# Kernel tuning notes

Hardware: AMD Instinct MI355X
Metric: run time of the kernel (lower is better)

Reference implementation:

```python
import jax, jax.numpy as jnp
import numpy as np

B, N, IN_DIM = 256, 300, 1280
DIM, DEPTH, HEADS = 256, 2, 4
DIM_HEAD = DIM // HEADS            # 64
NB_FEAT = int(DIM_HEAD * np.log(DIM_HEAD))  # 266, lucidrains default
FF_HIDDEN = 4 * DIM
LN_EPS = 1e-5
KERNEL_EPS = 1e-4


def _orthogonal_random_matrix(nb_rows, nb_cols, rng):
    # gaussian orthogonal random matrix, scaling=0 (chi-norm multipliers)
    blocks = []
    full = nb_rows // nb_cols
    for _ in range(full):
        q, _ = np.linalg.qr(rng.standard_normal((nb_cols, nb_cols)))
        blocks.append(q.T)
    rem = nb_rows - full * nb_cols
    if rem:
        q, _ = np.linalg.qr(rng.standard_normal((nb_cols, nb_cols)))
        blocks.append(q.T[:rem])
    mat = np.concatenate(blocks, 0)
    mult = np.linalg.norm(rng.standard_normal((nb_rows, nb_cols)), axis=1)
    return (mult[:, None] * mat).astype(np.float32)


def setup_inputs() -> dict:
    key = jax.random.key(0)
    ks = jax.random.split(key, 24)
    s = 0.02
    rng = np.random.default_rng(0)
    proj = jnp.asarray(np.stack([_orthogonal_random_matrix(NB_FEAT, DIM_HEAD, rng)
                                 for _ in range(DEPTH)]))  # [L, M, dh]
    return {
        "x": jax.random.normal(ks[0], (B, N, IN_DIM), jnp.float32),
        "w_in": jax.random.normal(ks[1], (IN_DIM, DIM), jnp.float32) * s,
        "b_in": jnp.zeros((DIM,), jnp.float32),
        "proj": proj,
        "ln1_g": jnp.ones((DEPTH, DIM), jnp.float32),
        "ln1_b": jnp.zeros((DEPTH, DIM), jnp.float32),
        "wq": jax.random.normal(ks[2], (DEPTH, DIM, DIM), jnp.float32) * s,
        "wk": jax.random.normal(ks[3], (DEPTH, DIM, DIM), jnp.float32) * s,
        "wv": jax.random.normal(ks[4], (DEPTH, DIM, DIM), jnp.float32) * s,
        "wo": jax.random.normal(ks[5], (DEPTH, DIM, DIM), jnp.float32) * s,
        "bo": jnp.zeros((DEPTH, DIM), jnp.float32),
        "ln2_g": jnp.ones((DEPTH, DIM), jnp.float32),
        "ln2_b": jnp.zeros((DEPTH, DIM), jnp.float32),
        "w1": jax.random.normal(ks[6], (DEPTH, DIM, FF_HIDDEN), jnp.float32) * s,
        "b1": jnp.zeros((DEPTH, FF_HIDDEN), jnp.float32),
        "w2": jax.random.normal(ks[7], (DEPTH, FF_HIDDEN, DIM), jnp.float32) * s,
        "b2": jnp.zeros((DEPTH, DIM), jnp.float32),
        "hln_g": jnp.ones((DIM,), jnp.float32),
        "hln_b": jnp.zeros((DIM,), jnp.float32),
        "wh1": jax.random.normal(ks[8], (DIM, 128), jnp.float32) * s,
        "bh1": jnp.zeros((128,), jnp.float32),
        "wh2": jax.random.normal(ks[9], (128, 1), jnp.float32) * s,
        "bh2": jnp.zeros((1,), jnp.float32),
    }


def _layernorm(x, g, b):
    mu = jnp.mean(x, -1, keepdims=True)
    var = jnp.mean(jnp.square(x - mu), -1, keepdims=True)
    return (x - mu) * jax.lax.rsqrt(var + LN_EPS) * g + b


def _softmax_kernel(data, proj, is_query):
    # data: [b,h,n,dh], proj: [m,dh] -> features [b,h,n,m] (FAVOR+ positive softmax kernel)
    norm = DIM_HEAD ** -0.25
    ratio = proj.shape[0] ** -0.5
    dd = jnp.einsum('bhnd,md->bhnm', data * norm, proj)
    diag = 0.5 * jnp.sum(jnp.square(data), -1) * (norm ** 2)  # [b,h,n]
    if is_query:
        stab = jnp.max(dd, axis=-1, keepdims=True)
    else:
        stab = jnp.max(dd, axis=(-2, -1), keepdims=True)
    return ratio * (jnp.exp(dd - diag[..., None] - stab) + KERNEL_EPS)


def _linear_attention(q, k, v, proj):
    # non-causal FAVOR+: O(n*m*d) instead of O(n^2*d)
    qp = _softmax_kernel(q, proj, True)    # [b,h,n,m]
    kp = _softmax_kernel(k, proj, False)   # [b,h,n,m]
    d_inv = 1.0 / jnp.einsum('bhnm,bhm->bhn', qp, jnp.sum(kp, axis=-2))
    context = jnp.einsum('bhnm,bhnd->bhmd', kp, v)
    return jnp.einsum('bhnm,bhmd->bhnd', qp, context) * d_inv[..., None]


def reference(x, w_in, b_in, proj, ln1_g, ln1_b, wq, wk, wv, wo, bo,
              ln2_g, ln2_b, w1, b1, w2, b2, hln_g, hln_b, wh1, bh1, wh2, bh2):
    h = x @ w_in + b_in                                   # [B,N,DIM]
    for l in range(DEPTH):
        # --- pre-norm FAVOR+ self-attention ---
        y = _layernorm(h, ln1_g[l], ln1_b[l])
        q = (y @ wq[l]).reshape(B, N, HEADS, DIM_HEAD).transpose(0, 2, 1, 3)
        k = (y @ wk[l]).reshape(B, N, HEADS, DIM_HEAD).transpose(0, 2, 1, 3)
        v = (y @ wv[l]).reshape(B, N, HEADS, DIM_HEAD).transpose(0, 2, 1, 3)
        o = _linear_attention(q, k, v, proj[l])
        o = o.transpose(0, 2, 1, 3).reshape(B, N, DIM)
        h = h + (o @ wo[l] + bo[l])
        # --- pre-norm FFN (GELU, mult=4) ---
        y = _layernorm(h, ln2_g[l], ln2_b[l])
        h = h + (jax.nn.gelu(y @ w1[l] + b1[l]) @ w2[l] + b2[l])
    pooled = jnp.mean(h, axis=1)                          # [B,DIM]
    z = _layernorm(pooled, hln_g, hln_b)
    z = jax.nn.relu(z @ wh1 + bh1)
    return jax.nn.sigmoid(z @ wh2 + bh2)                  # [B,1]
```

## Files before the change

kernel.cpp:

```cpp
#include <hip/hip_runtime.h>
#include <hip/hip_bf16.h>


#define MF 266
#define NSEQ 300
#define DIMC 256
#define NORM_QK 0.3535533905932738f
#define KEPS 1e-4f

typedef __attribute__((ext_vector_type(8))) short bf16x8;
typedef __attribute__((ext_vector_type(4))) float f32x4;

#define MFMA16(a, b, c) __builtin_amdgcn_mfma_f32_16x16x32_bf16((a), (b), (c), 0, 0, 0)

__device__ __forceinline__ float bfbits2f(ushort u) {
  return __uint_as_float(((unsigned int)u) << 16);
}
__device__ __forceinline__ ushort f2us(float f) {
  __hip_bfloat16 b = __float2bfloat16(f);
  return *(ushort*)&b;
}
__device__ __forceinline__ float sq8(uint4 u) {
  float s = 0.f;
  const unsigned int uu[4] = {u.x, u.y, u.z, u.w};
#pragma unroll
  for (int i = 0; i < 4; i++) {
    const float a = bfbits2f((ushort)(uu[i] & 0xffff));
    const float b = bfbits2f((ushort)(uu[i] >> 16));
    s += a * a + b * b;
  }
  return s;
}
__device__ __forceinline__ void gld16(const void* g, void* l) {
  __builtin_amdgcn_global_load_lds(
      (const __attribute__((address_space(1))) unsigned int*)g,
      (__attribute__((address_space(3))) unsigned int*)l, 16, 0, 0);
}
__device__ __forceinline__ float fast_gelu(float x) {
  const float t = 0.7978845608028654f * (x + 0.044715f * x * x * x);
  const float e = __expf(2.0f * fabsf(t));
  float th = 1.0f - 2.0f / (e + 1.0f);
  th = (t < 0.0f) ? -th : th;
  return 0.5f * x * (1.0f + th);
}

template<int EPI, int OUTBF, int AF32>
__global__ __launch_bounds__(256) void gemm_mfma(
    const ushort* __restrict__ A, const float* __restrict__ Af,
    const ushort* __restrict__ BT,
    const float* __restrict__ bias, const float* __restrict__ R,
    float* __restrict__ Cf, __hip_bfloat16* __restrict__ Cb,
    ushort* __restrict__ Cq, int M, int N, int K)
{
  __shared__ ushort As[128][32];
  __shared__ ushort Bs[128][32];
  const int tid = threadIdx.x;
  const int row0 = blockIdx.x << 7, col0 = blockIdx.y << 7;
  const int w = tid >> 6, lane = tid & 63;
  const int wm = (w >> 1) << 6, wn = (w & 1) << 6;
  const int r = lane & 15, quad = lane >> 4;
  const int sr = tid >> 2, sc = (tid & 3) << 3;
  f32x4 acc[4][4];
#pragma unroll
  for (int i = 0; i < 4; i++)
#pragma unroll
    for (int j = 0; j < 4; j++) acc[i][j] = (f32x4){0.f, 0.f, 0.f, 0.f};
  const ushort* ap0 = A + (size_t)(row0 + sr) * K + sc;
  const ushort* ap1 = A + (size_t)(row0 + sr + 64) * K + sc;
  const float*  af0 = Af + (size_t)(row0 + sr) * K + sc;
  const float*  af1 = Af + (size_t)(row0 + sr + 64) * K + sc;
  const ushort* bp0 = BT + (size_t)(col0 + sr) * K + sc;
  const ushort* bp1 = BT + (size_t)(col0 + sr + 64) * K + sc;
  for (int k0 = 0; k0 < K; k0 += 32) {
    if (AF32) {
      const float4 u0 = *(const float4*)(af0 + k0);
      const float4 u1 = *(const float4*)(af0 + k0 + 4);
      const float4 u2 = *(const float4*)(af1 + k0);
      const float4 u3 = *(const float4*)(af1 + k0 + 4);
      ushort4 p0, p1, p2, p3;
      p0.x=f2us(u0.x); p0.y=f2us(u0.y); p0.z=f2us(u0.z); p0.w=f2us(u0.w);
      p1.x=f2us(u1.x); p1.y=f2us(u1.y); p1.z=f2us(u1.z); p1.w=f2us(u1.w);
      p2.x=f2us(u2.x); p2.y=f2us(u2.y); p2.z=f2us(u2.z); p2.w=f2us(u2.w);
      p3.x=f2us(u3.x); p3.y=f2us(u3.y); p3.z=f2us(u3.z); p3.w=f2us(u3.w);
      *(ushort4*)&As[sr][sc]      = p0;
      *(ushort4*)&As[sr][sc+4]    = p1;
      *(ushort4*)&As[sr+64][sc]   = p2;
      *(ushort4*)&As[sr+64][sc+4] = p3;
    } else {
      gld16(ap0 + k0, &As[sr][sc]);
      gld16(ap1 + k0, &As[sr + 64][sc]);
    }
    gld16(bp0 + k0, &Bs[sr][sc]);
    gld16(bp1 + k0, &Bs[sr + 64][sc]);
    __syncthreads();
    bf16x8 af[4], bfv[4];
#pragma unroll
    for (int i = 0; i < 4; i++) af[i]  = *(const bf16x8*)&As[wm + i*16 + r][quad << 3];
#pragma unroll
    for (int i = 0; i < 4; i++) bfv[i] = *(const bf16x8*)&Bs[wn + i*16 + r][quad << 3];
#pragma unroll
    for (int mi = 0; mi < 4; mi++)
#pragma unroll
      for (int ni = 0; ni < 4; ni++)
        acc[mi][ni] = MFMA16(af[mi], bfv[ni], acc[mi][ni]);
    __syncthreads();
  }
#pragma unroll
  for (int mi = 0; mi < 4; mi++) {
    const int rowb = row0 + wm + mi*16 + (quad << 2);
#pragma unroll
    for (int ni = 0; ni < 4; ni++) {
      const int col = col0 + wn + ni*16 + r;
      if (EPI == 4) {
        const int tsel = col >> 8, hd = col & 255, hh = hd >> 6, d = hd & 63;
        const float sc_ = (tsel == 2) ? 1.f : NORM_QK;
#pragma unroll
        for (int j = 0; j < 4; j++) {
          const int rowj = rowb + j;
          const int bq = rowj / 300, nq = rowj - bq * 300;
          Cq[(((size_t)tsel * 1024 + (bq << 2) + hh) * 300 + nq) * 64 + d] =
              f2us(acc[mi][ni][j] * sc_);
        }
      } else {
        const float bv = bias[col];
#pragma unroll
        for (int j = 0; j < 4; j++) {
          const size_t off = (size_t)(rowb + j) * N + col;
          float vv = acc[mi][ni][j] + bv;
          if (EPI == 1) vv += R[off];
          if (EPI == 2) vv = fast_gelu(vv);
          if (OUTBF) Cb[off] = __float2bfloat16(vv);
          else       Cf[off] = vv;
        }
      }
    }
  }
}

__global__ __launch_bounds__(256) void cast_bf16_kernel(
    const float* __restrict__ in, ushort* __restrict__ out, int n4)
{
  const int i = blockIdx.x * 256 + threadIdx.x;
  if (i >= n4) return;
  const float4 v = ((const float4*)in)[i];
  ushort4 rr;
  rr.x = f2us(v.x); rr.y = f2us(v.y); rr.z = f2us(v.z); rr.w = f2us(v.w);
  ((ushort4*)out)[i] = rr;
}

struct TSeg { const float* src; ushort* dst; int R; int C; int base; };
struct TTab { TSeg s[13]; };
__global__ __launch_bounds__(256) void tcast_all(TTab tab) {
  __shared__ float t[32][33];
  const int bid = blockIdx.x;
  int si = 0;
#pragma unroll
  for (int i = 1; i < 13; i++) if (bid >= tab.s[i].base) si = i;
  const float* src = tab.s[si].src;
  ushort* dst = tab.s[si].dst;
  const int R = tab.s[si].R, C = tab.s[si].C;
  const int local = bid - tab.s[si].base;
  const int cw = C >> 5;
  const int c0 = (local % cw) << 5, r0 = (local / cw) << 5;
  const int tx = threadIdx.x & 31, ty = threadIdx.x >> 5;
#pragma unroll
  for (int i = 0; i < 32; i += 8)
    t[ty + i][tx] = src[(size_t)(r0 + ty + i) * C + c0 + tx];
  __syncthreads();
#pragma unroll
  for (int i = 0; i < 32; i += 8)
    dst[(size_t)(c0 + ty + i) * R + r0 + tx] = f2us(t[tx][ty + i]);
}

__global__ __launch_bounds__(256) void ln_kernel(
    const float* __restrict__ x, const float* __restrict__ g,
    const float* __restrict__ b, __hip_bfloat16* __restrict__ y)
{
  const int wid = threadIdx.x >> 6, lane = threadIdx.x & 63;
  const int row = blockIdx.x * 4 + wid;
  const float* xr = x + (size_t)row * DIMC;
  float v[4];
  float s = 0.f;
#pragma unroll
  for (int i = 0; i < 4; i++) { v[i] = xr[lane + 64*i]; s += v[i]; }
#pragma unroll
  for (int off = 32; off; off >>= 1) s += __shfl_xor(s, off);
  const float mu = s * (1.0f/256.0f);
  float var = 0.f;
#pragma unroll
  for (int i = 0; i < 4; i++) { const float d = v[i] - mu; var += d*d; }
#pragma unroll
  for (int off = 32; off; off >>= 1) var += __shfl_xor(var, off);
  const float rstd = rsqrtf(var * (1.0f/256.0f) + 1e-5f);
  __hip_bfloat16* yr = y + (size_t)row * DIMC;
#pragma unroll
  for (int i = 0; i < 4; i++) {
    const int c = lane + 64*i;
    yr[c] = __float2bfloat16((v[i] - mu) * rstd * g[c] + b[c]);
  }
}

__global__ __launch_bounds__(512) void favor_fused_kernel(
    const ushort* __restrict__ qn_all, const ushort* __restrict__ kn_all,
    const ushort* __restrict__ v_all, const ushort* __restrict__ projb,
    ushort* __restrict__ Ob)
{
  __shared__ __align__(16) uint8_t smem[151424];
  ushort (*kn_s)[72]      = (ushort(*)[72])(smem);
  ushort (*vT_s)[328]     = (ushort(*)[328])(smem + 46080);
  ushort (*proj_s)[72]    = (ushort(*)[72])(smem + 88064);
  ushort (*kpT_s)[40]     = (ushort(*)[40])(smem + 127232);
  ushort (*qp_s)[16][72]  = (ushort(*)[16][72])(smem + 127232);
  float* diag_s = (float*)(smem + 148992);
  float* ksum_s = (float*)(smem + 150272);
  float* red_s  = (float*)(smem + 151360);

  const int tid = threadIdx.x, w = tid >> 6, lane = tid & 63;
  const int bh = blockIdx.x;
  const int b = bh >> 2, h = bh & 3;
  const int r = lane & 15, quad = lane >> 4;
  const int rl = lane >> 3, c8 = lane & 7;

  {
    const ushort* knb = kn_all + (size_t)bh * 19200;
    for (int row = w*8 + rl; row < 320; row += 64) {
      uint4 u = {0u,0u,0u,0u};
      if (row < 300) u = *(const uint4*)(knb + row*64 + c8*8);
      *(uint4*)&kn_s[row][c8*8] = u;
      float s = sq8(u);
      s += __shfl_xor(s, 1); s += __shfl_xor(s, 2); s += __shfl_xor(s, 4);
      if (c8 == 0) diag_s[row] = 0.5f * s;
    }
    const ushort* vb = v_all + (size_t)bh * 19200;
    for (int row = w*8 + rl; row < 328; row += 64) {
      uint4 u = {0u,0u,0u,0u};
      if (row < 300) u = *(const uint4*)(vb + row*64 + c8*8);
      const unsigned int uu[4] = {u.x, u.y, u.z, u.w};
#pragma unroll
      for (int p = 0; p < 4; p++) {
        vT_s[c8*8 + 2*p    ][row] = (ushort)(uu[p] & 0xffff);
        vT_s[c8*8 + 2*p + 1][row] = (ushort)(uu[p] >> 16);
      }
    }
    for (int row = w*8 + rl; row < 272; row += 64) {
      uint4 u = {0u,0u,0u,0u};
      if (row < 266) u = *(const uint4*)(projb + row*64 + c8*8);
      *(uint4*)&proj_s[row][c8*8] = u;
    }
  }
  __syncthreads();

  f32x4 cacc[9];
#pragma unroll
  for (int i = 0; i < 9; i++) cacc[i] = (f32x4){0.f,0.f,0.f,0.f};
  float ksum_acc = 0.f;
  float stab = -3.0e38f;

  for (int c = 0; c < 10; c++) {
    f32x4 ddreg[5];
    float cmax = -3.0e38f;
#pragma unroll
    for (int ii = 0; ii < 5; ii++) {
      const int t = w + ii*8;
      if (t < 34) {
        const int tm = t >> 1, tn = c*2 + (t & 1);
        const bf16x8 a0 = *(const bf16x8*)&proj_s[tm*16 + r][quad*8];
        const bf16x8 a1 = *(const bf16x8*)&proj_s[tm*16 + r][32 + quad*8];
        const bf16x8 b0 = *(const bf16x8*)&kn_s[tn*16 + r][quad*8];
        const bf16x8 b1 = *(const bf16x8*)&kn_s[tn*16 + r][32 + quad*8];
        f32x4 acc = (f32x4){0.f,0.f,0.f,0.f};
        acc = MFMA16(a0, b0, acc);
        acc = MFMA16(a1, b1, acc);
        ddreg[ii] = acc;
        const int n = tn*16 + r;
        if (n < 300) {
#pragma unroll
          for (int j = 0; j < 4; j++) {
            const int m = tm*16 + quad*4 + j;
            if (m < 266) cmax = fmaxf(cmax, acc[j]);
          }
        }
      }
    }
#pragma unroll
    for (int off = 32; off; off >>= 1) cmax = fmaxf(cmax, __shfl_xor(cmax, off));
    if (lane == 0) red_s[w] = cmax;
    __syncthreads();
    float bmax = red_s[0];
#pragma unroll
    for (int i = 1; i < 8; i++) bmax = fmaxf(bmax, red_s[i]);
    const float stab_new = fmaxf(stab, bmax);
    const float alpha = __expf(stab - stab_new);
    stab = stab_new;
    ksum_acc *= alpha;
#pragma unroll
    for (int i = 0; i < 9; i++)
#pragma unroll
      for (int j = 0; j < 4; j++) cacc[i][j] *= alpha;
#pragma unroll
    for (int ii = 0; ii < 5; ii++) {
      const int t = w + ii*8;
      if (t < 34) {
        const int tm = t >> 1, tnl = t & 1, tn = c*2 + tnl;
        const int n = tn*16 + r;
        const float dgn = diag_s[n];
#pragma unroll
        for (int j = 0; j < 4; j++) {
          const int m = tm*16 + quad*4 + j;
          float kp = 0.f;
          if (n < 300 && m < 266) kp = __expf(ddreg[ii][j] - dgn - stab) + KEPS;
          kpT_s[m][tnl*16 + r] = f2us(kp);
        }
      }
    }
    __syncthreads();
    if (tid < 272) {
      float rs = 0.f;
#pragma unroll
      for (int kk = 0; kk < 4; kk++) {
        const uint4 u = *(const uint4*)&kpT_s[tid][kk*8];
        const unsigned int uu[4] = {u.x, u.y, u.z, u.w};
#pragma unroll
        for (int p = 0; p < 4; p++)
          rs += bfbits2f((ushort)(uu[p] & 0xffff)) + bfbits2f((ushort)(uu[p] >> 16));
      }
      ksum_acc += rs;
    }
#pragma unroll
    for (int ii = 0; ii < 9; ii++) {
      const int t2 = w + ii*8;
      if (t2 < 68) {
        const int tm = t2 >> 2, td = t2 & 3;
        const bf16x8 aa = *(const bf16x8*)&kpT_s[tm*16 + r][quad*8];
        const bf16x8 bb = *(const bf16x8*)&vT_s[td*16 + r][c*32 + quad*8];
        cacc[ii] = MFMA16(aa, bb, cacc[ii]);
      }
    }
    __syncthreads();
  }

  if (tid < 272) ksum_s[tid] = ksum_acc;
#pragma unroll
  for (int ii = 0; ii < 9; ii++) {
    const int t2 = w + ii*8;
    if (t2 < 68) {
      const int tm = t2 >> 2, td = t2 & 3;
#pragma unroll
      for (int j = 0; j < 4; j++) {
        const int m = tm*16 + quad*4 + j;
        vT_s[td*16 + r][m] = f2us(cacc[ii][j]);
      }
    }
  }
  {
    const ushort* qb = qn_all + (size_t)bh * 19200;
    for (int row = w*8 + rl; row < 320; row += 64) {
      uint4 u = {0u,0u,0u,0u};
      if (row < 300) u = *(const uint4*)(qb + row*64 + c8*8);
      *(uint4*)&kn_s[row][c8*8] = u;
      float s = sq8(u);
      s += __shfl_xor(s, 1); s += __shfl_xor(s, 2); s += __shfl_xor(s, 4);
      if (c8 == 0) diag_s[row] = 0.5f * s;
    }
  }
  __syncthreads();

  for (int t = w; t < 19; t += 8) {
    const bf16x8 a0 = *(const bf16x8*)&kn_s[t*16 + r][quad*8];
    const bf16x8 a1 = *(const bf16x8*)&kn_s[t*16 + r][32 + quad*8];
    f32x4 dd[17];
#pragma unroll
    for (int tm = 0; tm < 17; tm++) {
      const bf16x8 b0 = *(const bf16x8*)&proj_s[tm*16 + r][quad*8];
      const bf16x8 b1 = *(const bf16x8*)&proj_s[tm*16 + r][32 + quad*8];
      f32x4 acc = (f32x4){0.f,0.f,0.f,0.f};
      acc = MFMA16(a0, b0, acc);
      acc = MFMA16(a1, b1, acc);
      dd[tm] = acc;
    }
    float mxj[4] = {-3.0e38f, -3.0e38f, -3.0e38f, -3.0e38f};
#pragma unroll
    for (int tm = 0; tm < 17; tm++) {
      if (tm*16 + r < 266) {
#pragma unroll
        for (int j = 0; j < 4; j++) mxj[j] = fmaxf(mxj[j], dd[tm][j]);
      }
    }
#pragma unroll
    for (int off = 1; off < 16; off <<= 1)
#pragma unroll
      for (int j = 0; j < 4; j++) mxj[j] = fmaxf(mxj[j], __shfl_xor(mxj[j], off));
    float dg[4];
#pragma unroll
    for (int j = 0; j < 4; j++) dg[j] = diag_s[t*16 + quad*4 + j];
    float den[4] = {0.f, 0.f, 0.f, 0.f};
#pragma unroll
    for (int tm = 0; tm < 17; tm++) {
      const float ks = ksum_s[tm*16 + r];
      const bool mval = (tm*16 + r < 266);
#pragma unroll
      for (int j = 0; j < 4; j++) {
        const int n = t*16 + quad*4 + j;
        float qp = 0.f;
        if (mval && n < 300) qp = __expf(dd[tm][j] - dg[j] - mxj[j]) + KEPS;
        dd[tm][j] = qp;
        den[j] += qp * ks;
      }
    }
#pragma unroll
    for (int off = 1; off < 16; off <<= 1)
#pragma unroll
      for (int j = 0; j < 4; j++) den[j] += __shfl_xor(den[j], off);
    float dinv[4];
#pragma unroll
    for (int j = 0; j < 4; j++) dinv[j] = 1.0f / den[j];

    f32x4 oacc[4];
#pragma unroll
    for (int td = 0; td < 4; td++) oacc[td] = (f32x4){0.f,0.f,0.f,0.f};
#pragma unroll
    for (int g = 0; g < 5; g++) {
#pragma unroll
      for (int tt = 0; tt < 4; tt++) {
        const int tm = g*4 + tt;
#pragma unroll
        for (int j = 0; j < 4; j++) {
          const ushort us = (tm <= 16) ? f2us(dd[tm][j]) : (ushort)0;
          qp_s[w][quad*4 + j][tt*16 + r] = us;
        }
      }
#pragma unroll
      for (int s = 0; s < 2; s++) {
        const bf16x8 aa = *(const bf16x8*)&qp_s[w][r][s*32 + quad*8];
#pragma unroll
        for (int td = 0; td < 4; td++) {
          const bf16x8 bb = *(const bf16x8*)&vT_s[td*16 + r][g*64 + s*32 + quad*8];
          oacc[td] = MFMA16(aa, bb, oacc[td]);
        }
      }
    }
#pragma unroll
    for (int td = 0; td < 4; td++) {
#pragma unroll
      for (int j = 0; j < 4; j++) {
        const int n = t*16 + quad*4 + j;
        if (n < 300)
          Ob[((size_t)b*300 + n)*256 + h*64 + td*16 + r] = f2us(oacc[td][j] * dinv[j]);
      }
    }
  }
}

__global__ __launch_bounds__(256) void head_kernel(
    const float* __restrict__ h, const float* __restrict__ hg,
    const float* __restrict__ hb, const float* __restrict__ wh1,
    const float* __restrict__ bh1, const float* __restrict__ wh2,
    const float* __restrict__ bh2, float* __restrict__ out)
{
  __shared__ float z_s[256];
  __shared__ float hid_s[128];
  __shared__ float red_s[4];
  const int b = blockIdx.x, tid = threadIdx.x;
  const float* hb_ = h + (size_t)b * NSEQ * DIMC;
  float s = 0.f;
  for (int n = 0; n < NSEQ; n++) s += hb_[(size_t)n * DIMC + tid];
  s *= (1.0f / 300.0f);
  float t1 = s;
#pragma unroll
  for (int off = 32; off; off >>= 1) t1 += __shfl_xor(t1, off);
  if ((tid & 63) == 0) red_s[tid >> 6] = t1;
  __syncthreads();
  const float mu = (red_s[0] + red_s[1] + red_s[2] + red_s[3]) * (1.0f/256.0f);
  __syncthreads();
  const float d = s - mu;
  float vv = d * d;
#pragma unroll
  for (int off = 32; off; off >>= 1) vv += __shfl_xor(vv, off);
  if ((tid & 63) == 0) red_s[tid >> 6] = vv;
  __syncthreads();
  const float var = (red_s[0] + red_s[1] + red_s[2] + red_s[3]) * (1.0f/256.0f);
  z_s[tid] = d * rsqrtf(var + 1e-5f) * hg[tid] + hb[tid];
  __syncthreads();
  if (tid < 128) {
    float acc = bh1[tid];
    for (int dd = 0; dd < 256; dd++) acc += z_s[dd] * wh1[dd * 128 + tid];
    hid_s[tid] = fmaxf(acc, 0.f);
  }
  __syncthreads();
  if (tid < 64) {
    float acc = hid_s[tid] * wh2[tid] + hid_s[tid + 64] * wh2[tid + 64];
#pragma unroll
    for (int off = 32; off; off >>= 1) acc += __shfl_xor(acc, off);
    if (tid == 0) {
      const float val = acc + bh2[0];
      out[b] = 1.0f / (1.0f + __expf(-val));
    }
  }
}

extern "C" void kernel_launch(void* const* d_in, const int* in_sizes, int n_in,
                              void* d_out, int out_size, void* d_ws, size_t ws_size,
                              hipStream_t stream) {
  const float* x    = (const float*)d_in[0];
  const float* w_in = (const float*)d_in[1];
  const float* b_in = (const float*)d_in[2];
  const float* proj = (const float*)d_in[3];
  const float* ln1g = (const float*)d_in[4];
  const float* ln1b = (const float*)d_in[5];
  const float* wq   = (const float*)d_in[6];
  const float* wk   = (const float*)d_in[7];
  const float* wv   = (const float*)d_in[8];
  const float* wo   = (const float*)d_in[9];
  const float* bo   = (const float*)d_in[10];
  const float* ln2g = (const float*)d_in[11];
  const float* ln2b = (const float*)d_in[12];
  const float* w1   = (const float*)d_in[13];
  const float* b1   = (const float*)d_in[14];
  const float* w2   = (const float*)d_in[15];
  const float* b2   = (const float*)d_in[16];
  const float* hg   = (const float*)d_in[17];
  const float* hbp  = (const float*)d_in[18];
  const float* wh1  = (const float*)d_in[19];
  const float* bh1  = (const float*)d_in[20];
  const float* wh2  = (const float*)d_in[21];
  const float* bh2  = (const float*)d_in[22];

  uint8_t* base = (uint8_t*)d_ws;
  float*  h     = (float*)(base);
  ushort* yb    = (ushort*)(base + 78643200);
  ushort* qkv   = (ushort*)(base + 117964800);
  ushort* ob    = (ushort*)(base + 235929600);
  ushort* wbuf  = (ushort*)(base + 275251200);
  ushort* projb = (ushort*)(base + 279052288);
  ushort* tb = qkv;
  ushort* qb = qkv;
  ushort* kb = qkv + 19660800;
  ushort* vb = qkv + 39321600;

  ushort* w_inT = wbuf;
  ushort* wT0   = wbuf + 327680;

  cast_bf16_kernel<<<34, 256, 0, stream>>>(proj, projb, 8512);
  TTab tab;
  int nb = 0;
  auto add = [&](const float* s, ushort* d, int R, int C) {
    tab.s[nb % 13] = TSeg{s, d, R, C, 0};
  };
  {
    int idx = 0, basem = 0;
    auto seg = [&](const float* s, ushort* d, int R, int C) {
      tab.s[idx] = TSeg{s, d, R, C, basem};
      basem += (R >> 5) * (C >> 5);
      idx++;
    };
    seg(w_in, w_inT, 1280, 256);
    for (int l = 0; l < 2; l++) {
      ushort* wl = wT0 + (size_t)l * 786432;
      seg(wq + (size_t)l*65536,  wl,          256, 256);
      seg(wk + (size_t)l*65536,  wl + 65536,  256, 256);
      seg(wv + (size_t)l*65536,  wl + 131072, 256, 256);
      seg(wo + (size_t)l*65536,  wl + 196608, 256, 256);
      seg(w1 + (size_t)l*262144, wl + 262144, 256, 1024);
      seg(w2 + (size_t)l*262144, wl + 524288, 1024, 256);
    }
    nb = basem;
  }
  tcast_all<<<nb, 256, 0, stream>>>(tab);

  gemm_mfma<0,0,1><<<dim3(600, 2), 256, 0, stream>>>(
      nullptr, x, w_inT, b_in, nullptr, h, nullptr, nullptr, 76800, 256, 1280);

  for (int l = 0; l < 2; l++) {
    ushort* wl = wT0 + (size_t)l * 786432;
    ushort* projL = projb + (size_t)l * 17024;
    ln_kernel<<<19200, 256, 0, stream>>>(h, ln1g + l*256, ln1b + l*256, (__hip_bfloat16*)yb);
    gemm_mfma<4,0,0><<<dim3(600, 6), 256, 0, stream>>>(
        yb, nullptr, wl, nullptr, nullptr, nullptr, nullptr, qkv, 76800, 768, 256);
    favor_fused_kernel<<<1024, 512, 0, stream>>>(qb, kb, vb, projL, ob);
    gemm_mfma<1,0,0><<<dim3(600, 2), 256, 0, stream>>>(
        ob, nullptr, wl + 196608, bo + l*256, h, h, nullptr, nullptr, 76800, 256, 256);
    ln_kernel<<<19200, 256, 0, stream>>>(h, ln2g + l*256, ln2b + l*256, (__hip_bfloat16*)yb);
    gemm_mfma<2,1,0><<<dim3(600, 8), 256, 0, stream>>>(
        yb, nullptr, wl + 262144, b1 + l*1024, nullptr, nullptr, (__hip_bfloat16*)tb, nullptr, 76800, 1024, 256);
    gemm_mfma<1,0,0><<<dim3(600, 2), 256, 0, stream>>>(
        tb, nullptr, wl + 524288, b2 + l*256, h, h, nullptr, nullptr, 76800, 256, 1024);
  }
  head_kernel<<<256, 256, 0, stream>>>(h, hg, hbp, wh1, bh1, wh2, bh2, (float*)d_out);
}
```

Measured before the change: 1.790 ms.

## Fuse LN2, FFN up-projection with GELU, and down-projection into one kernel

```diff
diff --git a/kernel.cpp b/kernel.cpp
--- a/kernel.cpp
+++ b/kernel.cpp
@@ -55,7 +55,7 @@
   __shared__ ushort As[128][32];
   __shared__ ushort Bs[128][32];
   const int tid = threadIdx.x;
-  const int row0 = blockIdx.x << 7, col0 = blockIdx.y << 7;
+  const int row0 = blockIdx.y << 7, col0 = blockIdx.x << 7;
   const int w = tid >> 6, lane = tid & 63;
   const int wm = (w >> 1) << 6, wn = (w & 1) << 6;
   const int r = lane & 15, quad = lane >> 4;
@@ -128,10 +128,131 @@
           const size_t off = (size_t)(rowb + j) * N + col;
           float vv = acc[mi][ni][j] + bv;
           if (EPI == 1) vv += R[off];
-          if (EPI == 2) vv = fast_gelu(vv);
           if (OUTBF) Cb[off] = __float2bfloat16(vv);
           else       Cf[off] = vv;
         }
+      }
+    }
+  }
+}
+
+__global__ __launch_bounds__(512, 4) void ffn_fused_kernel(
+    float* __restrict__ h, const ushort* __restrict__ w1T,
+    const float* __restrict__ b1, const ushort* __restrict__ w2T,
+    const float* __restrict__ b2, const float* __restrict__ lng,
+    const float* __restrict__ lnb)
+{
+  __shared__ ushort Ys[64][264];
+  __shared__ ushort Hs[64][136];
+  const int tid = threadIdx.x, w = tid >> 6, lane = tid & 63;
+  const int r = lane & 15, quad = lane >> 4;
+  const int row0 = blockIdx.x << 6;
+
+  {
+    const int rl = lane >> 3, c8 = lane & 7;
+    const int row = (w << 3) + rl;
+    const float4* h4 = (const float4*)(h + (size_t)(row0 + row) * DIMC);
+    float4 v[8];
+    float s = 0.f;
+#pragma unroll
+    for (int g = 0; g < 8; g++) {
+      v[g] = h4[g*8 + c8];
+      s += v[g].x + v[g].y + v[g].z + v[g].w;
+    }
+    s += __shfl_xor(s, 1); s += __shfl_xor(s, 2); s += __shfl_xor(s, 4);
+    const float mu = s * (1.0f/256.0f);
+    float var = 0.f;
+#pragma unroll
+    for (int g = 0; g < 8; g++) {
+      const float a=v[g].x-mu, b=v[g].y-mu, c=v[g].z-mu, d=v[g].w-mu;
+      var += a*a + b*b + c*c + d*d;
+    }
+    var += __shfl_xor(var, 1); var += __shfl_xor(var, 2); var += __shfl_xor(var, 4);
+    const float rstd = rsqrtf(var * (1.0f/256.0f) + 1e-5f);
+#pragma unroll
+    for (int g = 0; g < 8; g++) {
+      const int col = (g*8 + c8) << 2;
+      const float4 gg = *(const float4*)(lng + col);
+      const float4 bb = *(const float4*)(lnb + col);
+      ushort4 o;
+      o.x = f2us((v[g].x - mu) * rstd * gg.x + bb.x);
+      o.y = f2us((v[g].y - mu) * rstd * gg.y + bb.y);
+      o.z = f2us((v[g].z - mu) * rstd * gg.z + bb.z);
+      o.w = f2us((v[g].w - mu) * rstd * gg.w + bb.w);
+      *(ushort4*)&Ys[row][col] = o;
+    }
+  }
+  __syncthreads();
+
+  const int kb = (w & 3) << 5, mb = (w >> 2) << 5;
+  const int mo = mb, no = (w & 3) << 6;
+
+  f32x4 oacc[2][4];
+#pragma unroll
+  for (int i = 0; i < 2; i++)
+#pragma unroll
+    for (int j = 0; j < 4; j++) oacc[i][j] = (f32x4){0.f, 0.f, 0.f, 0.f};
+
+  for (int nc = 0; nc < 8; nc++) {
+    f32x4 hacc[2][2];
+#pragma unroll
+    for (int i = 0; i < 2; i++)
+#pragma unroll
+      for (int j = 0; j < 2; j++) hacc[i][j] = (f32x4){0.f, 0.f, 0.f, 0.f};
+    const ushort* w1p = w1T + (size_t)(nc*128 + kb + r) * 256 + (quad << 3);
+#pragma unroll
+    for (int ks = 0; ks < 8; ks++) {
+      const int k0 = ks << 5;
+      const bf16x8 a0 = *(const bf16x8*)(w1p + k0);
+      const bf16x8 a1 = *(const bf16x8*)(w1p + 16*256 + k0);
+      const bf16x8 y0 = *(const bf16x8*)&Ys[mb + r][k0 + (quad << 3)];
+      const bf16x8 y1 = *(const bf16x8*)&Ys[mb + 16 + r][k0 + (quad << 3)];
+      hacc[0][0] = MFMA16(a0, y0, hacc[0][0]);
+      hacc[0][1] = MFMA16(a0, y1, hacc[0][1]);
+      hacc[1][0] = MFMA16(a1, y0, hacc[1][0]);
+      hacc[1][1] = MFMA16(a1, y1, hacc[1][1]);
+    }
+#pragma unroll
+    for (int i = 0; i < 2; i++) {
+      const int khb = kb + i*16 + (quad << 2);
+      const float4 bv = *(const float4*)(b1 + nc*128 + khb);
+#pragma unroll
+      for (int j = 0; j < 2; j++) {
+        ushort4 hv;
+        hv.x = f2us(fast_gelu(hacc[i][j][0] + bv.x));
+        hv.y = f2us(fast_gelu(hacc[i][j][1] + bv.y));
+        hv.z = f2us(fast_gelu(hacc[i][j][2] + bv.z));
+        hv.w = f2us(fast_gelu(hacc[i][j][3] + bv.w));
+        *(ushort4*)&Hs[mb + j*16 + r][khb] = hv;
+      }
+    }
+    __syncthreads();
+#pragma unroll
+    for (int kq = 0; kq < 4; kq++) {
+      const bf16x8 a0 = *(const bf16x8*)&Hs[mo + r][kq*32 + (quad << 3)];
+      const bf16x8 a1 = *(const bf16x8*)&Hs[mo + 16 + r][kq*32 + (quad << 3)];
+#pragma unroll
+      for (int jn = 0; jn < 4; jn++) {
+        const bf16x8 bb = *(const bf16x8*)(
+            w2T + (size_t)(no + jn*16 + r) * 1024 + nc*128 + kq*32 + (quad << 3));
+        oacc[0][jn] = MFMA16(a0, bb, oacc[0][jn]);
+        oacc[1][jn] = MFMA16(a1, bb, oacc[1][jn]);
+      }
+    }
+    __syncthreads();
+  }
+
+#pragma unroll
+  for (int i = 0; i < 2; i++) {
+    const int mbase = row0 + mo + i*16 + (quad << 2);
+#pragma unroll
+    for (int jn = 0; jn < 4; jn++) {
+      const int n = no + jn*16 + r;
+      const float b2v = b2[n];
+#pragma unroll
+      for (int jj = 0; jj < 4; jj++) {
+        float* hp = h + (size_t)(mbase + jj) * DIMC + n;
+        *hp += oacc[i][jn][jj] + b2v;
       }
     }
   }
@@ -532,7 +653,6 @@
   ushort* ob    = (ushort*)(base + 235929600);
   ushort* wbuf  = (ushort*)(base + 275251200);
   ushort* projb = (ushort*)(base + 279052288);
-  ushort* tb = qkv;
   ushort* qb = qkv;
   ushort* kb = qkv + 19660800;
   ushort* vb = qkv + 39321600;
@@ -543,9 +663,6 @@
   cast_bf16_kernel<<<34, 256, 0, stream>>>(proj, projb, 8512);
   TTab tab;
   int nb = 0;
-  auto add = [&](const float* s, ushort* d, int R, int C) {
-    tab.s[nb % 13] = TSeg{s, d, R, C, 0};
-  };
   {
     int idx = 0, basem = 0;
     auto seg = [&](const float* s, ushort* d, int R, int C) {
@@ -567,23 +684,21 @@
   }
   tcast_all<<<nb, 256, 0, stream>>>(tab);
 
-  gemm_mfma<0,0,1><<<dim3(600, 2), 256, 0, stream>>>(
+  gemm_mfma<0,0,1><<<dim3(2, 600), 256, 0, stream>>>(
       nullptr, x, w_inT, b_in, nullptr, h, nullptr, nullptr, 76800, 256, 1280);
 
   for (int l = 0; l < 2; l++) {
     ushort* wl = wT0 + (size_t)l * 786432;
     ushort* projL = projb + (size_t)l * 17024;
     ln_kernel<<<19200, 256, 0, stream>>>(h, ln1g + l*256, ln1b + l*256, (__hip_bfloat16*)yb);
-    gemm_mfma<4,0,0><<<dim3(600, 6), 256, 0, stream>>>(
+    gemm_mfma<4,0,0><<<dim3(6, 600), 256, 0, stream>>>(
         yb, nullptr, wl, nullptr, nullptr, nullptr, nullptr, qkv, 76800, 768, 256);
     favor_fused_kernel<<<1024, 512, 0, stream>>>(qb, kb, vb, projL, ob);
-    gemm_mfma<1,0,0><<<dim3(600, 2), 256, 0, stream>>>(
+    gemm_mfma<1,0,0><<<dim3(2, 600), 256, 0, stream>>>(
         ob, nullptr, wl + 196608, bo + l*256, h, h, nullptr, nullptr, 76800, 256, 256);
-    ln_kernel<<<19200, 256, 0, stream>>>(h, ln2g + l*256, ln2b + l*256, (__hip_bfloat16*)yb);
-    gemm_mfma<2,1,0><<<dim3(600, 8), 256, 0, stream>>>(
-        yb, nullptr, wl + 262144, b1 + l*1024, nullptr, nullptr, (__hip_bfloat16*)tb, nullptr, 76800, 1024, 256);
-    gemm_mfma<1,0,0><<<dim3(600, 2), 256, 0, stream>>>(
-        tb, nullptr, wl + 524288, b2 + l*256, h, h, nullptr, nullptr, 76800, 256, 1024);
+    ffn_fused_kernel<<<1200, 512, 0, stream>>>(
+        h, wl + 262144, b1 + (size_t)l*1024, wl + 524288, b2 + (size_t)l*256,
+        ln2g + l*256, ln2b + l*256);
   }
   head_kernel<<<256, 256, 0, stream>>>(h, hg, hbp, wh1, bh1, wh2, bh2, (float*)d_out);
 }
```

Result: slower. 1.991 ms (+11.2%).
